# Optimization experiments

Hardware: AMD Instinct MI355X
Metric: run time of the kernel (lower is better)

## Reference

```python
import jax, jax.numpy as jnp
import numpy as np

H = 8          # num heads
LN_EPS = 1e-5  # torch LayerNorm default

_SHAPES = {
    'src': (1024, 8, 256), 'pos': (1024, 8, 256), 'query_embed': (80, 8, 256), 'cam_mask': (8, 80, 1024),
    'enc_qkv_w': (2, 768, 256), 'enc_qkv_b': (2, 768), 'enc_out_w': (2, 256, 256), 'enc_out_b': (2, 256),
    'enc_ln1_g': (2, 256), 'enc_ln1_b': (2, 256),
    'enc_ff1_w': (2, 2048, 256), 'enc_ff1_b': (2, 2048), 'enc_ff2_w': (2, 256, 2048), 'enc_ff2_b': (2, 256),
    'enc_ln2_g': (2, 256), 'enc_ln2_b': (2, 256),
    'dec_sa_qkv_w': (2, 768, 256), 'dec_sa_qkv_b': (2, 768), 'dec_sa_out_w': (2, 256, 256), 'dec_sa_out_b': (2, 256),
    'dec_ln1_g': (2, 256), 'dec_ln1_b': (2, 256),
    'dec_ca_qkv_w': (2, 768, 256), 'dec_ca_qkv_b': (2, 768), 'dec_ca_out_w': (2, 256, 256), 'dec_ca_out_b': (2, 256),
    'dec_ln2_g': (2, 256), 'dec_ln2_b': (2, 256),
    'dec_ff1_w': (2, 2048, 256), 'dec_ff1_b': (2, 2048), 'dec_ff2_w': (2, 256, 2048), 'dec_ff2_b': (2, 256),
    'dec_ln3_g': (2, 256), 'dec_ln3_b': (2, 256),
    'dec_norm_g': (256,), 'dec_norm_b': (256,),
}


def setup_inputs() -> dict:
    key = jax.random.key(0)
    out = {}
    for i, (name, sh) in enumerate(_SHAPES.items()):
        k = jax.random.fold_in(key, i)
        if name.endswith('_g'):
            out[name] = jnp.ones(sh, jnp.float32)
        elif name.endswith('ln1_b') or name.endswith('ln2_b') or name.endswith('ln3_b') or name == 'dec_norm_b':
            out[name] = jnp.zeros(sh, jnp.float32)
        else:
            scale = 1.0 if name in ('src', 'pos', 'query_embed', 'cam_mask') else 0.02
            out[name] = jax.random.normal(k, sh, dtype=jnp.float32) * scale
    return out


def layer_norm(x, g, b):
    mu = jnp.mean(x, axis=-1, keepdims=True)
    var = jnp.mean(jnp.square(x - mu), axis=-1, keepdims=True)
    return (x - mu) * jax.lax.rsqrt(var + LN_EPS) * g + b


def mha(q_in, k_in, v_in, qkv_w, qkv_b, out_w, out_b, bias=None):
    # q_in: [L,B,D], k_in/v_in: [S,B,D]; torch layout: projections are x @ W.T + b
    L, B, D = q_in.shape
    S = k_in.shape[0]
    hd = D // H
    wq, wk, wv = qkv_w[:D], qkv_w[D:2 * D], qkv_w[2 * D:]
    bq, bk, bv = qkv_b[:D], qkv_b[D:2 * D], qkv_b[2 * D:]
    q = (q_in @ wq.T + bq).reshape(L, B, H, hd).transpose(1, 2, 0, 3)  # [B,H,L,hd]
    k = (k_in @ wk.T + bk).reshape(S, B, H, hd).transpose(1, 2, 0, 3)  # [B,H,S,hd]
    v = (v_in @ wv.T + bv).reshape(S, B, H, hd).transpose(1, 2, 0, 3)
    logits = jnp.einsum('bhld,bhsd->bhls', q, k) * (1.0 / np.sqrt(hd))
    if bias is not None:
        logits = logits + bias[:, None, :, :]  # CAM bias broadcast over heads
    attn = jax.nn.softmax(logits, axis=-1)
    o = jnp.einsum('bhls,bhsd->bhld', attn, v).transpose(2, 0, 1, 3).reshape(L, B, D)
    return o @ out_w.T + out_b


def reference(src, pos, query_embed, cam_mask,
              enc_qkv_w, enc_qkv_b, enc_out_w, enc_out_b, enc_ln1_g, enc_ln1_b,
              enc_ff1_w, enc_ff1_b, enc_ff2_w, enc_ff2_b, enc_ln2_g, enc_ln2_b,
              dec_sa_qkv_w, dec_sa_qkv_b, dec_sa_out_w, dec_sa_out_b, dec_ln1_g, dec_ln1_b,
              dec_ca_qkv_w, dec_ca_qkv_b, dec_ca_out_w, dec_ca_out_b, dec_ln2_g, dec_ln2_b,
              dec_ff1_w, dec_ff1_b, dec_ff2_w, dec_ff2_b, dec_ln3_g, dec_ln3_b,
              dec_norm_g, dec_norm_b):
    n_enc = enc_qkv_w.shape[0]
    n_dec = dec_sa_qkv_w.shape[0]
    # --- encoder (post-norm DETR style, pos added to q,k) ---
    mem = src
    for i in range(n_enc):
        qk = mem + pos
        a = mha(qk, qk, mem, enc_qkv_w[i], enc_qkv_b[i], enc_out_w[i], enc_out_b[i])
        mem = layer_norm(mem + a, enc_ln1_g[i], enc_ln1_b[i])
        f = jax.nn.relu(mem @ enc_ff1_w[i].T + enc_ff1_b[i]) @ enc_ff2_w[i].T + enc_ff2_b[i]
        mem = layer_norm(mem + f, enc_ln2_g[i], enc_ln2_b[i])
    # --- decoder: tgt starts at zeros (Q2L), query_embed is query_pos ---
    tgt = jnp.zeros_like(query_embed)
    for i in range(n_dec):
        qk = tgt + query_embed
        sa = mha(qk, qk, tgt, dec_sa_qkv_w[i], dec_sa_qkv_b[i], dec_sa_out_w[i], dec_sa_out_b[i])
        tgt = layer_norm(tgt + sa, dec_ln1_g[i], dec_ln1_b[i])
        ca = mha(tgt + query_embed, mem + pos, mem,
                 dec_ca_qkv_w[i], dec_ca_qkv_b[i], dec_ca_out_w[i], dec_ca_out_b[i],
                 bias=cam_mask)  # MA: CAM-derived additive attention bias [B,L,S]
        tgt = layer_norm(tgt + ca, dec_ln2_g[i], dec_ln2_b[i])
        f = jax.nn.relu(tgt @ dec_ff1_w[i].T + dec_ff1_b[i]) @ dec_ff2_w[i].T + dec_ff2_b[i]
        tgt = layer_norm(tgt + f, dec_ln3_g[i], dec_ln3_b[i])
    out = layer_norm(tgt, dec_norm_g, dec_norm_b)
    return out[None]  # [1, L, B, D] as in TransformerDecoder's output.unsqueeze(0)
```

## Files before the change

kernel.cpp:

```cpp
#include <hip/hip_runtime.h>
#include <hip/hip_bf16.h>
#include <cstdint>
#include <cstddef>

typedef __hip_bfloat16 bf16;
typedef float f4 __attribute__((ext_vector_type(4)));
typedef float f32x4 __attribute__((ext_vector_type(4)));
typedef short s8v __attribute__((ext_vector_type(8)));
typedef unsigned short u16x4 __attribute__((ext_vector_type(4)));

#define LN_EPS 1e-5f

__device__ __forceinline__ void async_cp16(const void* g, void* lds) {
  __builtin_amdgcn_global_load_lds(
      (const __attribute__((address_space(1))) unsigned int*)g,
      (__attribute__((address_space(3))) unsigned int*)lds, 16, 0, 0);
}

#define NCAST 11
struct CastArgs {
  const float* in[NCAST];
  bf16* out[NCAST];
  int end4[NCAST];
  int nseg;
};

__global__ __launch_bounds__(256) void cast_multi(CastArgs a, int total4) {
  int i = blockIdx.x * 256 + threadIdx.x;
  if (i >= total4) return;
  int s = 0;
  while (i >= a.end4[s]) ++s;
  int j = i - (s ? a.end4[s - 1] : 0);
  f4 v = ((const f4*)a.in[s])[j];
  u16x4 o;
#pragma unroll
  for (int c = 0; c < 4; ++c) {
    bf16 h = __float2bfloat16(v[c]);
    o[c] = *reinterpret_cast<unsigned short*>(&h);
  }
  ((u16x4*)a.out[s])[j] = o;
}

__global__ __launch_bounds__(256) void add_bf16_kernel(const float* __restrict__ a,
                                                       const float* __restrict__ b,
                                                       bf16* __restrict__ out, int n4) {
  int i = blockIdx.x * 256 + threadIdx.x;
  if (i < n4) {
    f4 x = ((const f4*)a)[i];
    f4 y = ((const f4*)b)[i];
    u16x4 o;
#pragma unroll
    for (int j = 0; j < 4; ++j) {
      bf16 h = __float2bfloat16(x[j] + y[j]);
      o[j] = *reinterpret_cast<unsigned short*>(&h);
    }
    ((u16x4*)out)[i] = o;
  }
}

template <int TB, int MODE, int SPLITK>
__global__ __launch_bounds__(256, 2) void mfma_gemm(
    const bf16* __restrict__ A, const bf16* __restrict__ W,
    const float* __restrict__ bias, float* __restrict__ C,
    bf16* __restrict__ Cb, int M, int N, int K, int HL) {
  constexpr int WM = TB / 2, WN = TB / 2;
  constexpr int MR = WM / 16, NR = WN / 16;
  constexpr int NCH = TB / 32;
  __shared__ __attribute__((aligned(16))) unsigned short As[TB][64];
  __shared__ __attribute__((aligned(16))) unsigned short Ws[TB][64];
  const int tid = threadIdx.x;
  const int lane = tid & 63, wave = tid >> 6;
  const int wr = wave >> 1, wc = wave & 1;
  const int bm = blockIdx.x * TB, bn = blockIdx.y * TB;
  const int fr = lane & 15, fo = lane >> 4;
  const int srowi = lane >> 3;
  const int slot = lane & 7;
  const int gcol = (slot ^ srowi) * 8;

  const int kchunk = K / SPLITK;
  const int kbeg = (SPLITK > 1) ? blockIdx.z * kchunk : 0;

  f32x4 acc[MR][NR] = {};

  for (int k0 = kbeg; k0 < kbeg + kchunk; k0 += 64) {
    __syncthreads();
#pragma unroll
    for (int c = 0; c < NCH; ++c) {
      int rbase = wave * (TB / 4) + c * 8;
      int row = rbase + srowi;
      async_cp16(A + (size_t)(bm + row) * K + k0 + gcol, &As[rbase][0]);
      async_cp16(W + (size_t)(bn + row) * K + k0 + gcol, &Ws[rbase][0]);
    }
    __syncthreads();
#pragma unroll
    for (int ks = 0; ks < 2; ++ks) {
      s8v a[MR], b[NR];
#pragma unroll
      for (int mi = 0; mi < MR; ++mi) {
        int row = wr * WM + mi * 16 + fr;
        a[mi] = *(const s8v*)((const char*)&As[0][0] + row * 128 +
                              ((ks * 64 + fo * 16) ^ ((row & 7) << 4)));
      }
#pragma unroll
      for (int ni = 0; ni < NR; ++ni) {
        int row = wc * WN + ni * 16 + fr;
        b[ni] = *(const s8v*)((const char*)&Ws[0][0] + row * 128 +
                              ((ks * 64 + fo * 16) ^ ((row & 7) << 4)));
      }
#pragma unroll
      for (int mi = 0; mi < MR; ++mi)
#pragma unroll
        for (int ni = 0; ni < NR; ++ni)
          acc[mi][ni] = __builtin_amdgcn_mfma_f32_16x16x32_bf16(
              a[mi], b[ni], acc[mi][ni], 0, 0, 0);
    }
  }

  const int r0 = (lane >> 4) * 4;
  float* Cz = (MODE == 4) ? C + (size_t)blockIdx.z * M * N : C;
#pragma unroll
  for (int mi = 0; mi < MR; ++mi) {
#pragma unroll
    for (int ni = 0; ni < NR; ++ni) {
      int col = bn + wc * WN + ni * 16 + fr;
      float bv = (MODE == 4) ? 0.f : bias[col];
#pragma unroll
      for (int r = 0; r < 4; ++r) {
        int row = bm + wr * WM + mi * 16 + r0 + r;
        float t = acc[mi][ni][r] + bv;
        if (MODE == 2) t = fmaxf(t, 0.f);
        if (MODE == 0) {
          C[(size_t)row * N + col] = t;
        } else if (MODE == 4) {
          Cz[(size_t)row * N + col] = t;
        } else if (MODE == 3) {
          int l = row >> 3, bb = row & 7;
          int sec = col >> 8, hh = (col >> 5) & 7, d = col & 31;
          Cb[(size_t)sec * ((size_t)64 * HL * 32) +
             ((size_t)(bb * 8 + hh) * HL + l) * 32 + d] = __float2bfloat16(t);
        } else {
          Cb[(size_t)row * N + col] = __float2bfloat16(t);
        }
      }
    }
  }
}

template <int HAS_BIAS, int PARTIAL>
__global__ __launch_bounds__(256) void attn_mfma(
    const bf16* __restrict__ Qh, const bf16* __restrict__ Kh,
    const bf16* __restrict__ Vh, const float* __restrict__ bias,
    bf16* __restrict__ O, float* __restrict__ PO, float* __restrict__ PM,
    float* __restrict__ PL, int L, int S, int SC, float scale) {
  __shared__ __attribute__((aligned(16))) unsigned short Ks[64][40];
  __shared__ __attribute__((aligned(16))) unsigned short Vt[32][88];
  __shared__ __attribute__((aligned(16))) unsigned short Ps[4][16][72];
  const int tid = threadIdx.x;
  const int lane = tid & 63, wave = tid >> 6;
  const int fr = lane & 15, fo = lane >> 4;
  const int bh = blockIdx.y;
  const int b = bh >> 3, h = bh & 7;
  const int q0 = blockIdx.x * 64 + wave * 16;

  const int cz = PARTIAL ? blockIdx.z : 0;
  const int sb = PARTIAL ? cz * SC : 0;
  const int se = PARTIAL ? min(S, sb + SC) : S;

  s8v qf = {};
  if (q0 + fr < L)
    qf = *(const s8v*)(Qh + ((size_t)bh * L + q0 + fr) * 32 + fo * 8);

  float m[4] = {-1e30f, -1e30f, -1e30f, -1e30f};
  float lsum[4] = {};
  f32x4 oacc[2] = {};

  const int srow = tid & 63, sco = (tid >> 6) * 8;
  const int qrow_base = q0 + fo * 4;

  s8v kvN = {}, vvN = {};
  auto load_tile = [&](int s0) {
    s8v kv = {}, vv = {};
    if (s0 + srow < se) {
      size_t so = ((size_t)bh * S + s0 + srow) * 32 + sco;
      kv = *(const s8v*)(Kh + so);
      vv = *(const s8v*)(Vh + so);
    }
    kvN = kv; vvN = vv;
  };
  auto store_tile = [&]() {
    *(s8v*)&Ks[srow][sco] = kvN;
#pragma unroll
    for (int j = 0; j < 8; ++j)
      Vt[sco + j][srow] = ((unsigned short*)&vvN)[j];
  };

  load_tile(sb);
  store_tile();
  __syncthreads();

  for (int s0 = sb; s0 < se; s0 += 64) {
    const bool more = (s0 + 64 < se);
    if (more) load_tile(s0 + 64);

    f32x4 sa[4];
#pragma unroll
    for (int kb = 0; kb < 4; ++kb) {
      s8v bf = *(const s8v*)&Ks[kb * 16 + fr][fo * 8];
      f32x4 z = {};
      sa[kb] = __builtin_amdgcn_mfma_f32_16x16x32_bf16(qf, bf, z, 0, 0, 0);
    }

    float lg[4][4];
#pragma unroll
    for (int kb = 0; kb < 4; ++kb) {
      int key = s0 + kb * 16 + fr;
      bool kok = key < se;
#pragma unroll
      for (int r = 0; r < 4; ++r) {
        float t = sa[kb][r] * scale;
        if (HAS_BIAS) {
          int q = qrow_base + r;
          int qc = q < L ? q : L - 1;
          t += bias[((size_t)b * L + qc) * S + key];
        }
        lg[kb][r] = kok ? t : -1e30f;
      }
    }

    float tm[4];
#pragma unroll
    for (int r = 0; r < 4; ++r)
      tm[r] = fmaxf(fmaxf(lg[0][r], lg[1][r]), fmaxf(lg[2][r], lg[3][r]));
#pragma unroll
    for (int off = 1; off <= 8; off <<= 1)
#pragma unroll
      for (int r = 0; r < 4; ++r)
        tm[r] = fmaxf(tm[r], __shfl_xor(tm[r], off, 64));

    float pr[4][4];
#pragma unroll
    for (int r = 0; r < 4; ++r) {
      float nm = fmaxf(m[r], tm[r]);
      float rs = __expf(m[r] - nm);
      m[r] = nm;
      lsum[r] *= rs;
      oacc[0][r] *= rs;
      oacc[1][r] *= rs;
      float ps = 0.f;
#pragma unroll
      for (int kb = 0; kb < 4; ++kb) {
        float p = __expf(lg[kb][r] - nm);
        pr[kb][r] = p;
        ps += p;
      }
      lsum[r] += ps;
    }

#pragma unroll
    for (int kb = 0; kb < 4; ++kb)
#pragma unroll
      for (int r = 0; r < 4; ++r) {
        bf16 hp = __float2bfloat16(pr[kb][r]);
        Ps[wave][fo * 4 + r][kb * 16 + fr] = *(unsigned short*)&hp;
      }

#pragma unroll
    for (int ks = 0; ks < 2; ++ks) {
      s8v af = *(const s8v*)&Ps[wave][fr][ks * 32 + fo * 8];
#pragma unroll
      for (int dh = 0; dh < 2; ++dh) {
        s8v vf = *(const s8v*)&Vt[dh * 16 + fr][ks * 32 + fo * 8];
        oacc[dh] = __builtin_amdgcn_mfma_f32_16x16x32_bf16(af, vf, oacc[dh], 0, 0, 0);
      }
    }

    if (more) {
      __syncthreads();
      store_tile();
      __syncthreads();
    }
  }

#pragma unroll
  for (int off = 1; off <= 8; off <<= 1)
#pragma unroll
    for (int r = 0; r < 4; ++r)
      lsum[r] += __shfl_xor(lsum[r], off, 64);

#pragma unroll
  for (int r = 0; r < 4; ++r) {
    int q = qrow_base + r;
    if (q < L) {
      if (PARTIAL) {
        size_t pi = ((size_t)cz * 64 + bh) * L + q;
        float* po = PO + pi * 32;
        po[fr] = oacc[0][r];
        po[16 + fr] = oacc[1][r];
        if (fr == 0) { PM[pi] = m[r]; PL[pi] = lsum[r]; }
      } else {
        float inv = 1.f / lsum[r];
        bf16* op = O + ((size_t)q * 8 + b) * 256 + h * 32;
        op[fr] = __float2bfloat16(oacc[0][r] * inv);
        op[16 + fr] = __float2bfloat16(oacc[1][r] * inv);
      }
    }
  }
}

__global__ __launch_bounds__(256) void attn_combine(
    const float* __restrict__ PO, const float* __restrict__ PM,
    const float* __restrict__ PL, bf16* __restrict__ O, int L, int NC) {
  int gid = blockIdx.x * 256 + threadIdx.x;
  if (gid >= 64 * L * 32) return;
  int d = gid & 31;
  int rem = gid >> 5;
  int q = rem % L, bh = rem / L;
  int b = bh >> 3, h = bh & 7;
  float M = -1e30f;
  for (int c = 0; c < NC; ++c) M = fmaxf(M, PM[((size_t)c * 64 + bh) * L + q]);
  float lsum = 0.f, o = 0.f;
  for (int c = 0; c < NC; ++c) {
    size_t pi = ((size_t)c * 64 + bh) * L + q;
    float w = __expf(PM[pi] - M);
    lsum += PL[pi] * w;
    o += PO[pi * 32 + d] * w;
  }
  O[((size_t)q * 8 + b) * 256 + h * 32 + d] = __float2bfloat16(o / lsum);
}

__global__ __launch_bounds__(256) void ln_kernel(
    const float* __restrict__ x, const float* __restrict__ res,
    const float* __restrict__ parts, int nparts, int pstride,
    const float* __restrict__ gbias,
    const float* __restrict__ g, const float* __restrict__ b,
    float* __restrict__ out, bf16* __restrict__ outb) {
  const int row = blockIdx.x, tid = threadIdx.x;
  size_t idx = (size_t)row * 256 + tid;
  float v = x[idx];
  if (res) v += res[idx];
  if (parts) {
    for (int z = 0; z < nparts; ++z) v += parts[(size_t)z * pstride + idx];
  }
  if (gbias) v += gbias[tid];
  float s = v, s2 = v * v;
#pragma unroll
  for (int off = 32; off >= 1; off >>= 1) {
    s += __shfl_down(s, off);
    s2 += __shfl_down(s2, off);
  }
  __shared__ float red[8];
  int wv = tid >> 6;
  if ((tid & 63) == 0) { red[wv] = s; red[4 + wv] = s2; }
  __syncthreads();
  if (tid == 0) {
    float ts = red[0] + red[1] + red[2] + red[3];
    float ts2 = red[4] + red[5] + red[6] + red[7];
    float mu = ts * (1.f / 256.f);
    float var = ts2 * (1.f / 256.f) - mu * mu;
    red[0] = mu;
    red[1] = rsqrtf(var + LN_EPS);
  }
  __syncthreads();
  float y = (v - red[0]) * red[1] * g[tid] + b[tid];
  if (out) out[idx] = y;
  if (outb) outb[idx] = __float2bfloat16(y);
}

extern "C" void kernel_launch(void* const* d_in, const int* in_sizes, int n_in,
                              void* d_out, int out_size, void* d_ws, size_t ws_size,
                              hipStream_t stream) {
  const float* src         = (const float*)d_in[0];
  const float* pos         = (const float*)d_in[1];
  const float* query_embed = (const float*)d_in[2];
  const float* cam_mask    = (const float*)d_in[3];
  const float* enc_qkv_w   = (const float*)d_in[4];
  const float* enc_qkv_b   = (const float*)d_in[5];
  const float* enc_out_w   = (const float*)d_in[6];
  const float* enc_out_b   = (const float*)d_in[7];
  const float* enc_ln1_g   = (const float*)d_in[8];
  const float* enc_ln1_b   = (const float*)d_in[9];
  const float* enc_ff1_w   = (const float*)d_in[10];
  const float* enc_ff1_b   = (const float*)d_in[11];
  const float* enc_ff2_w   = (const float*)d_in[12];
  const float* enc_ff2_b   = (const float*)d_in[13];
  const float* enc_ln2_g   = (const float*)d_in[14];
  const float* enc_ln2_b   = (const float*)d_in[15];
  const float* dec_sa_qkv_w= (const float*)d_in[16];
  const float* dec_sa_qkv_b= (const float*)d_in[17];
  const float* dec_sa_out_w= (const float*)d_in[18];
  const float* dec_sa_out_b= (const float*)d_in[19];
  const float* dec_ln1_g   = (const float*)d_in[20];
  const float* dec_ln1_b   = (const float*)d_in[21];
  const float* dec_ca_qkv_w= (const float*)d_in[22];
  const float* dec_ca_qkv_b= (const float*)d_in[23];
  const float* dec_ca_out_w= (const float*)d_in[24];
  const float* dec_ca_out_b= (const float*)d_in[25];
  const float* dec_ln2_g   = (const float*)d_in[26];
  const float* dec_ln2_b   = (const float*)d_in[27];
  const float* dec_ff1_w   = (const float*)d_in[28];
  const float* dec_ff1_b   = (const float*)d_in[29];
  const float* dec_ff2_w   = (const float*)d_in[30];
  const float* dec_ff2_b   = (const float*)d_in[31];
  const float* dec_ln3_g   = (const float*)d_in[32];
  const float* dec_ln3_b   = (const float*)d_in[33];
  const float* dec_norm_g  = (const float*)d_in[34];
  const float* dec_norm_b  = (const float*)d_in[35];

  size_t off = 0;
  char* base = (char*)d_ws;
  auto af = [&](size_t n) { float* p = (float*)(base + off); off += n * 4; return p; };
  auto ab = [&](size_t n) { bf16*  p = (bf16*)(base + off);  off += n * 2; return p; };

  float* mem  = af(2097152);
  float* r1   = af(2097152);
  float* PO   = af(8388608);
  float* pm   = af(262144);
  float* pl   = af(262144);
  float* tgt  = af(163840);
  float* tpr  = af(163840);
  bf16* memb  = ab(2097152);
  bf16* qkb   = ab(2097152);
  bf16* aob   = ab(2097152);
  bf16* ffb   = ab(16777216);
  bf16* bufQ  = ab(4194304);
  bf16* bufK  = ab(2097152);
  bf16* bufV  = ab(2097152);
  bf16* tgtb  = ab(163840);
  bf16* tqkb  = ab(163840);
  bf16* taob  = ab(163840);
  bf16* tffb  = ab(1310720);
  bf16* w_enc_qkv = ab(393216);
  bf16* w_enc_out = ab(131072);
  bf16* w_enc_ff1 = ab(1048576);
  bf16* w_enc_ff2 = ab(1048576);
  bf16* w_sa_qkv  = ab(393216);
  bf16* w_sa_out  = ab(131072);
  bf16* w_ca_qkv  = ab(393216);
  bf16* w_ca_out  = ab(131072);
  bf16* w_dec_ff1 = ab(1048576);
  bf16* w_dec_ff2 = ab(1048576);

  const float scale = 0.17677669529663687f;

  {
    CastArgs ca;
    const float* ins[NCAST] = {enc_qkv_w, enc_out_w, enc_ff1_w, enc_ff2_w,
                               dec_sa_qkv_w, dec_sa_out_w, dec_ca_qkv_w,
                               dec_ca_out_w, dec_ff1_w, dec_ff2_w, src};
    bf16* outs[NCAST] = {w_enc_qkv, w_enc_out, w_enc_ff1, w_enc_ff2,
                         w_sa_qkv, w_sa_out, w_ca_qkv,
                         w_ca_out, w_dec_ff1, w_dec_ff2, memb};
    int n4s[NCAST] = {98304, 32768, 262144, 262144, 98304, 32768, 98304,
                      32768, 262144, 262144, 524288};
    int acc = 0;
    for (int s = 0; s < NCAST; ++s) {
      ca.in[s] = ins[s]; ca.out[s] = outs[s];
      acc += n4s[s]; ca.end4[s] = acc;
    }
    ca.nseg = NCAST;
    cast_multi<<<(acc + 255) / 256, 256, 0, stream>>>(ca, acc);
  }
  hipMemcpyAsync(mem, src, (size_t)2097152 * 4, hipMemcpyDeviceToDevice, stream);

  auto g64_f = [&](const bf16* A, const bf16* W, const float* bias, float* C,
                   int M, int N, int K) {
    mfma_gemm<64, 0, 1><<<dim3(M / 64, N / 64), 256, 0, stream>>>(
        A, W, bias, C, nullptr, M, N, K, 0);
  };
  auto g64_head = [&](const bf16* A, const bf16* W, const float* bias, bf16* Cb,
                      int M, int N, int K, int HL) {
    mfma_gemm<64, 3, 1><<<dim3(M / 64, N / 64), 256, 0, stream>>>(
        A, W, bias, nullptr, Cb, M, N, K, HL);
  };
  auto g64_relu = [&](const bf16* A, const bf16* W, const float* bias, bf16* Cb,
                      int M, int N, int K) {
    mfma_gemm<64, 2, 1><<<dim3(M / 64, N / 64), 256, 0, stream>>>(
        A, W, bias, nullptr, Cb, M, N, K, 0);
  };
  auto g128_relu = [&](const bf16* A, const bf16* W, const float* bias, bf16* Cb,
                       int M, int N, int K) {
    mfma_gemm<128, 2, 1><<<dim3(M / 128, N / 128), 256, 0, stream>>>(
        A, W, bias, nullptr, Cb, M, N, K, 0);
  };

  for (int i = 0; i < 2; ++i) {
    const bf16* wq = w_enc_qkv + (size_t)i * 196608;
    const float* qkvb = enc_qkv_b + (size_t)i * 768;
    add_bf16_kernel<<<2048, 256, 0, stream>>>(mem, pos, qkb, 524288);
    g64_head(qkb, wq, qkvb, bufQ, 8192, 512, 256, 1024);
    g64_head(memb, wq + 131072, qkvb + 512, bufV, 8192, 256, 256, 1024);
    attn_mfma<0, 0><<<dim3(16, 64), 256, 0, stream>>>(
        bufQ, bufQ + 2097152, bufV, nullptr, aob, nullptr, nullptr, nullptr,
        1024, 1024, 0, scale);
    g64_f(aob, w_enc_out + (size_t)i * 65536, enc_out_b + i * 256, r1,
          8192, 256, 256);
    ln_kernel<<<8192, 256, 0, stream>>>(mem, r1, nullptr, 0, 0, nullptr,
                                        enc_ln1_g + i * 256, enc_ln1_b + i * 256,
                                        mem, memb);
    g128_relu(memb, w_enc_ff1 + (size_t)i * 524288, enc_ff1_b + i * 2048, ffb,
              8192, 2048, 256);
    mfma_gemm<128, 4, 4><<<dim3(64, 2, 4), 256, 0, stream>>>(
        ffb, w_enc_ff2 + (size_t)i * 524288, nullptr, PO, nullptr,
        8192, 256, 2048, 0);
    ln_kernel<<<8192, 256, 0, stream>>>(mem, nullptr, PO, 4, 2097152,
                                        enc_ff2_b + i * 256,
                                        enc_ln2_g + i * 256, enc_ln2_b + i * 256,
                                        mem, memb);
  }

  hipMemsetAsync(tgt, 0, (size_t)163840 * 4, stream);
  hipMemsetAsync(tgtb, 0, (size_t)163840 * 2, stream);
  add_bf16_kernel<<<2048, 256, 0, stream>>>(mem, pos, qkb, 524288);

  for (int i = 0; i < 2; ++i) {
    const bf16* wsa = w_sa_qkv + (size_t)i * 196608;
    const float* sab = dec_sa_qkv_b + (size_t)i * 768;
    const bf16* wca = w_ca_qkv + (size_t)i * 196608;
    const float* cab = dec_ca_qkv_b + (size_t)i * 768;

    add_bf16_kernel<<<160, 256, 0, stream>>>(tgt, query_embed, tqkb, 40960);
    g64_head(tqkb, wsa, sab, bufQ, 640, 512, 256, 80);
    g64_head(tgtb, wsa + 131072, sab + 512, bufV, 640, 256, 256, 80);
    attn_mfma<0, 0><<<dim3(2, 64), 256, 0, stream>>>(
        bufQ, bufQ + 163840, bufV, nullptr, taob, nullptr, nullptr, nullptr,
        80, 80, 0, scale);
    g64_f(taob, w_sa_out + (size_t)i * 65536, dec_sa_out_b + i * 256, tpr,
          640, 256, 256);
    ln_kernel<<<640, 256, 0, stream>>>(tgt, tpr, nullptr, 0, 0, nullptr,
                                       dec_ln1_g + i * 256, dec_ln1_b + i * 256,
                                       tgt, tgtb);
    add_bf16_kernel<<<160, 256, 0, stream>>>(tgt, query_embed, tqkb, 40960);
    g64_head(tqkb, wca, cab, bufQ, 640, 256, 256, 80);
    g64_head(qkb, wca + 65536, cab + 256, bufK, 8192, 256, 256, 1024);
    g64_head(memb, wca + 131072, cab + 512, bufV, 8192, 256, 256, 1024);
    attn_mfma<1, 1><<<dim3(2, 64, 8), 256, 0, stream>>>(
        bufQ, bufK, bufV, cam_mask, nullptr, PO, pm, pl,
        80, 1024, 128, scale);
    attn_combine<<<640, 256, 0, stream>>>(PO, pm, pl, taob, 80, 8);
    g64_f(taob, w_ca_out + (size_t)i * 65536, dec_ca_out_b + i * 256, tpr,
          640, 256, 256);
    ln_kernel<<<640, 256, 0, stream>>>(tgt, tpr, nullptr, 0, 0, nullptr,
                                       dec_ln2_g + i * 256, dec_ln2_b + i * 256,
                                       tgt, tgtb);
    g64_relu(tgtb, w_dec_ff1 + (size_t)i * 524288, dec_ff1_b + i * 2048, tffb,
             640, 2048, 256);
    mfma_gemm<64, 4, 4><<<dim3(10, 4, 4), 256, 0, stream>>>(
        tffb, w_dec_ff2 + (size_t)i * 524288, nullptr, PO, nullptr,
        640, 256, 2048, 0);
    ln_kernel<<<640, 256, 0, stream>>>(tgt, nullptr, PO, 4, 163840,
                                       dec_ff2_b + i * 256,
                                       dec_ln3_g + i * 256, dec_ln3_b + i * 256,
                                       tgt, tgtb);
  }

  ln_kernel<<<640, 256, 0, stream>>>(tgt, nullptr, nullptr, 0, 0, nullptr,
                                     dec_norm_g, dec_norm_b,
                                     (float*)d_out, nullptr);
}
```

Before: 433.5 us.

## Rework attention: transposed V layout, LDS-free K/V loads, log2-domain softmax

The V projection now writes head-transposed output, so the attention kernel reads K and V fragments straight from global memory into registers instead of staging them through LDS with block-level syncs. Scores are computed transposed (K as the A operand), and the softmax scale and log2(e) are folded into the Q projection epilogue and a pre-scaled copy of cam_mask, so exp2f replaces __expf. A lazy rescale skips the running-max correction unless the max grows by more than 8. Bias reads become vectorised float4 loads and outputs are stored as packed writes. The grid axes are swapped, occupancy bounds are raised, and an extra scale kernel and buffer are added per call.

```diff
diff --git a/kernel.cpp b/kernel.cpp
--- a/kernel.cpp
+++ b/kernel.cpp
@@ -10,11 +10,17 @@
 typedef unsigned short u16x4 __attribute__((ext_vector_type(4)));
 
 #define LN_EPS 1e-5f
+#define LOG2E 1.4426950408889634f
 
 __device__ __forceinline__ void async_cp16(const void* g, void* lds) {
   __builtin_amdgcn_global_load_lds(
       (const __attribute__((address_space(1))) unsigned int*)g,
       (__attribute__((address_space(3))) unsigned int*)lds, 16, 0, 0);
+}
+
+__device__ __forceinline__ uint32_t pkbf(float lo, float hi) {
+  bf16 a = __float2bfloat16(lo), c = __float2bfloat16(hi);
+  return (uint32_t)*(unsigned short*)&a | ((uint32_t)*(unsigned short*)&c << 16);
 }
 
 #define NCAST 11
@@ -41,6 +47,16 @@
   ((u16x4*)a.out[s])[j] = o;
 }
 
+__global__ __launch_bounds__(256) void scale_f32_kernel(const float* __restrict__ in,
+                                                        float* __restrict__ out,
+                                                        float s, int n4) {
+  int i = blockIdx.x * 256 + threadIdx.x;
+  if (i < n4) {
+    f4 v = ((const f4*)in)[i];
+    ((f4*)out)[i] = v * s;
+  }
+}
+
 __global__ __launch_bounds__(256) void add_bf16_kernel(const float* __restrict__ a,
                                                        const float* __restrict__ b,
                                                        bf16* __restrict__ out, int n4) {
@@ -62,7 +78,7 @@
 __global__ __launch_bounds__(256, 2) void mfma_gemm(
     const bf16* __restrict__ A, const bf16* __restrict__ W,
     const float* __restrict__ bias, float* __restrict__ C,
-    bf16* __restrict__ Cb, int M, int N, int K, int HL) {
+    bf16* __restrict__ Cb, int M, int N, int K, int HL, float qscale) {
   constexpr int WM = TB / 2, WN = TB / 2;
   constexpr int MR = WM / 16, NR = WN / 16;
   constexpr int NCH = TB / 32;
@@ -136,8 +152,13 @@
         } else if (MODE == 3) {
           int l = row >> 3, bb = row & 7;
           int sec = col >> 8, hh = (col >> 5) & 7, d = col & 31;
+          if (sec == 0) t *= qscale;
           Cb[(size_t)sec * ((size_t)64 * HL * 32) +
              ((size_t)(bb * 8 + hh) * HL + l) * 32 + d] = __float2bfloat16(t);
+        } else if (MODE == 5) {
+          int l = row >> 3, bb = row & 7;
+          int hh = (col >> 5) & 7, d = col & 31;
+          Cb[((size_t)(bb * 8 + hh) * 32 + d) * HL + l] = __float2bfloat16(t);
         } else {
           Cb[(size_t)row * N + col] = __float2bfloat16(t);
         }
@@ -147,161 +168,156 @@
 }
 
 template <int HAS_BIAS, int PARTIAL>
-__global__ __launch_bounds__(256) void attn_mfma(
+__global__ __launch_bounds__(256, 4) void attn_mfma(
     const bf16* __restrict__ Qh, const bf16* __restrict__ Kh,
-    const bf16* __restrict__ Vh, const float* __restrict__ bias,
+    const bf16* __restrict__ VhT, const float* __restrict__ bias,
     bf16* __restrict__ O, float* __restrict__ PO, float* __restrict__ PM,
-    float* __restrict__ PL, int L, int S, int SC, float scale) {
-  __shared__ __attribute__((aligned(16))) unsigned short Ks[64][40];
-  __shared__ __attribute__((aligned(16))) unsigned short Vt[32][88];
-  __shared__ __attribute__((aligned(16))) unsigned short Ps[4][16][72];
+    float* __restrict__ PL, int L, int S, int SC) {
+  __shared__ __attribute__((aligned(16))) uint32_t Ps2[4][16][36];
   const int tid = threadIdx.x;
   const int lane = tid & 63, wave = tid >> 6;
   const int fr = lane & 15, fo = lane >> 4;
-  const int bh = blockIdx.y;
+  const int bh = blockIdx.x;
   const int b = bh >> 3, h = bh & 7;
-  const int q0 = blockIdx.x * 64 + wave * 16;
+  const int q0 = blockIdx.y * 64 + wave * 16;
+  const int q = q0 + fr;
 
   const int cz = PARTIAL ? blockIdx.z : 0;
   const int sb = PARTIAL ? cz * SC : 0;
   const int se = PARTIAL ? min(S, sb + SC) : S;
 
   s8v qf = {};
-  if (q0 + fr < L)
-    qf = *(const s8v*)(Qh + ((size_t)bh * L + q0 + fr) * 32 + fo * 8);
-
-  float m[4] = {-1e30f, -1e30f, -1e30f, -1e30f};
-  float lsum[4] = {};
+  if (q < L) qf = *(const s8v*)(Qh + ((size_t)bh * L + q) * 32 + fo * 8);
+
+  const float* brow = nullptr;
+  if (HAS_BIAS) brow = bias + ((size_t)b * L + (q < L ? q : L - 1)) * S;
+
+  float m = -1e30f, lsum = 0.f;
   f32x4 oacc[2] = {};
 
-  const int srow = tid & 63, sco = (tid >> 6) * 8;
-  const int qrow_base = q0 + fo * 4;
-
-  s8v kvN = {}, vvN = {};
-  auto load_tile = [&](int s0) {
-    s8v kv = {}, vv = {};
-    if (s0 + srow < se) {
-      size_t so = ((size_t)bh * S + s0 + srow) * 32 + sco;
-      kv = *(const s8v*)(Kh + so);
-      vv = *(const s8v*)(Vh + so);
-    }
-    kvN = kv; vvN = vv;
-  };
-  auto store_tile = [&]() {
-    *(s8v*)&Ks[srow][sco] = kvN;
-#pragma unroll
-    for (int j = 0; j < 8; ++j)
-      Vt[sco + j][srow] = ((unsigned short*)&vvN)[j];
-  };
-
-  load_tile(sb);
-  store_tile();
-  __syncthreads();
+  s8v kf[4];
+#pragma unroll
+  for (int kb = 0; kb < 4; ++kb)
+    kf[kb] = *(const s8v*)(Kh + ((size_t)bh * S + sb + kb * 16 + fr) * 32 + fo * 8);
 
   for (int s0 = sb; s0 < se; s0 += 64) {
     const bool more = (s0 + 64 < se);
-    if (more) load_tile(s0 + 64);
+    s8v kn[4];
+    if (more) {
+#pragma unroll
+      for (int kb = 0; kb < 4; ++kb)
+        kn[kb] = *(const s8v*)(Kh + ((size_t)bh * S + s0 + 64 + kb * 16 + fr) * 32 + fo * 8);
+    }
+    s8v vf[2][2];
+#pragma unroll
+    for (int dh = 0; dh < 2; ++dh)
+#pragma unroll
+      for (int ks = 0; ks < 2; ++ks)
+        vf[dh][ks] = *(const s8v*)(VhT + ((size_t)bh * 32 + dh * 16 + fr) * S +
+                                   s0 + ks * 32 + fo * 8);
+    f4 bias4[4];
+    if (HAS_BIAS) {
+#pragma unroll
+      for (int kb = 0; kb < 4; ++kb)
+        bias4[kb] = *(const f4*)(brow + s0 + kb * 16 + 4 * fo);
+    }
 
     f32x4 sa[4];
 #pragma unroll
     for (int kb = 0; kb < 4; ++kb) {
-      s8v bf = *(const s8v*)&Ks[kb * 16 + fr][fo * 8];
       f32x4 z = {};
-      sa[kb] = __builtin_amdgcn_mfma_f32_16x16x32_bf16(qf, bf, z, 0, 0, 0);
-    }
-
-    float lg[4][4];
+      sa[kb] = __builtin_amdgcn_mfma_f32_16x16x32_bf16(kf[kb], qf, z, 0, 0, 0);
+    }
+
+    float lg[16];
+#pragma unroll
+    for (int kb = 0; kb < 4; ++kb)
+#pragma unroll
+      for (int r = 0; r < 4; ++r)
+        lg[kb * 4 + r] = HAS_BIAS ? sa[kb][r] + bias4[kb][r] : sa[kb][r];
+
+    if (s0 + 64 > se) {
+#pragma unroll
+      for (int kb = 0; kb < 4; ++kb)
+#pragma unroll
+        for (int r = 0; r < 4; ++r)
+          if (s0 + kb * 16 + 4 * fo + r >= se) lg[kb * 4 + r] = -1e30f;
+    }
+
+    float tm = lg[0];
+#pragma unroll
+    for (int i = 1; i < 16; ++i) tm = fmaxf(tm, lg[i]);
+    tm = fmaxf(tm, __shfl_xor(tm, 16));
+    tm = fmaxf(tm, __shfl_xor(tm, 32));
+
+    if (__any(tm > m + 8.f)) {
+      float nm = fmaxf(m, tm);
+      float rs = exp2f(m - nm);
+      m = nm;
+      lsum *= rs;
+#pragma unroll
+      for (int r = 0; r < 4; ++r) { oacc[0][r] *= rs; oacc[1][r] *= rs; }
+    }
+
+    float pr[16];
+    float ps = 0.f;
+#pragma unroll
+    for (int i = 0; i < 16; ++i) {
+      pr[i] = exp2f(lg[i] - m);
+      ps += pr[i];
+    }
+    lsum += ps;
+
 #pragma unroll
     for (int kb = 0; kb < 4; ++kb) {
-      int key = s0 + kb * 16 + fr;
-      bool kok = key < se;
-#pragma unroll
-      for (int r = 0; r < 4; ++r) {
-        float t = sa[kb][r] * scale;
-        if (HAS_BIAS) {
-          int q = qrow_base + r;
-          int qc = q < L ? q : L - 1;
-          t += bias[((size_t)b * L + qc) * S + key];
-        }
-        lg[kb][r] = kok ? t : -1e30f;
+      uint32_t w0 = pkbf(pr[kb * 4 + 0], pr[kb * 4 + 1]);
+      uint32_t w1 = pkbf(pr[kb * 4 + 2], pr[kb * 4 + 3]);
+      uint64_t w = (uint64_t)w0 | ((uint64_t)w1 << 32);
+      *(uint64_t*)&Ps2[wave][fr][kb * 8 + 2 * fo] = w;
+    }
+
+    s8v pf[2];
+#pragma unroll
+    for (int ks = 0; ks < 2; ++ks)
+      pf[ks] = *(const s8v*)&Ps2[wave][fr][ks * 16 + 4 * fo];
+
+#pragma unroll
+    for (int dh = 0; dh < 2; ++dh)
+#pragma unroll
+      for (int ks = 0; ks < 2; ++ks)
+        oacc[dh] = __builtin_amdgcn_mfma_f32_16x16x32_bf16(
+            vf[dh][ks], pf[ks], oacc[dh], 0, 0, 0);
+
+    if (more) {
+#pragma unroll
+      for (int kb = 0; kb < 4; ++kb) kf[kb] = kn[kb];
+    }
+  }
+
+  lsum += __shfl_xor(lsum, 16);
+  lsum += __shfl_xor(lsum, 32);
+
+  if (q < L) {
+    if (PARTIAL) {
+      size_t pi = ((size_t)cz * 64 + bh) * L + q;
+      float* po = PO + pi * 32;
+#pragma unroll
+      for (int dh = 0; dh < 2; ++dh) {
+        f4 t;
+#pragma unroll
+        for (int r = 0; r < 4; ++r) t[r] = oacc[dh][r];
+        *(f4*)(po + dh * 16 + 4 * fo) = t;
       }
-    }
-
-    float tm[4];
-#pragma unroll
-    for (int r = 0; r < 4; ++r)
-      tm[r] = fmaxf(fmaxf(lg[0][r], lg[1][r]), fmaxf(lg[2][r], lg[3][r]));
-#pragma unroll
-    for (int off = 1; off <= 8; off <<= 1)
-#pragma unroll
-      for (int r = 0; r < 4; ++r)
-        tm[r] = fmaxf(tm[r], __shfl_xor(tm[r], off, 64));
-
-    float pr[4][4];
-#pragma unroll
-    for (int r = 0; r < 4; ++r) {
-      float nm = fmaxf(m[r], tm[r]);
-      float rs = __expf(m[r] - nm);
-      m[r] = nm;
-      lsum[r] *= rs;
-      oacc[0][r] *= rs;
-      oacc[1][r] *= rs;
-      float ps = 0.f;
-#pragma unroll
-      for (int kb = 0; kb < 4; ++kb) {
-        float p = __expf(lg[kb][r] - nm);
-        pr[kb][r] = p;
-        ps += p;
-      }
-      lsum[r] += ps;
-    }
-
-#pragma unroll
-    for (int kb = 0; kb < 4; ++kb)
-#pragma unroll
-      for (int r = 0; r < 4; ++r) {
-        bf16 hp = __float2bfloat16(pr[kb][r]);
-        Ps[wave][fo * 4 + r][kb * 16 + fr] = *(unsigned short*)&hp;
-      }
-
-#pragma unroll
-    for (int ks = 0; ks < 2; ++ks) {
-      s8v af = *(const s8v*)&Ps[wave][fr][ks * 32 + fo * 8];
+      if (fo == 0) { PM[pi] = m; PL[pi] = lsum; }
+    } else {
+      float inv = 1.f / lsum;
+      bf16* op = O + ((size_t)q * 8 + b) * 256 + h * 32;
 #pragma unroll
       for (int dh = 0; dh < 2; ++dh) {
-        s8v vf = *(const s8v*)&Vt[dh * 16 + fr][ks * 32 + fo * 8];
-        oacc[dh] = __builtin_amdgcn_mfma_f32_16x16x32_bf16(af, vf, oacc[dh], 0, 0, 0);
-      }
-    }
-
-    if (more) {
-      __syncthreads();
-      store_tile();
-      __syncthreads();
-    }
-  }
-
-#pragma unroll
-  for (int off = 1; off <= 8; off <<= 1)
-#pragma unroll
-    for (int r = 0; r < 4; ++r)
-      lsum[r] += __shfl_xor(lsum[r], off, 64);
-
-#pragma unroll
-  for (int r = 0; r < 4; ++r) {
-    int q = qrow_base + r;
-    if (q < L) {
-      if (PARTIAL) {
-        size_t pi = ((size_t)cz * 64 + bh) * L + q;
-        float* po = PO + pi * 32;
-        po[fr] = oacc[0][r];
-        po[16 + fr] = oacc[1][r];
-        if (fr == 0) { PM[pi] = m[r]; PL[pi] = lsum[r]; }
-      } else {
-        float inv = 1.f / lsum[r];
-        bf16* op = O + ((size_t)q * 8 + b) * 256 + h * 32;
-        op[fr] = __float2bfloat16(oacc[0][r] * inv);
-        op[16 + fr] = __float2bfloat16(oacc[1][r] * inv);
+        uint32_t w0 = pkbf(oacc[dh][0] * inv, oacc[dh][1] * inv);
+        uint32_t w1 = pkbf(oacc[dh][2] * inv, oacc[dh][3] * inv);
+        *(uint32_t*)(op + dh * 16 + 4 * fo) = w0;
+        *(uint32_t*)(op + dh * 16 + 4 * fo + 2) = w1;
       }
     }
   }
@@ -321,7 +337,7 @@
   float lsum = 0.f, o = 0.f;
   for (int c = 0; c < NC; ++c) {
     size_t pi = ((size_t)c * 64 + bh) * L + q;
-    float w = __expf(PM[pi] - M);
+    float w = exp2f(PM[pi] - M);
     lsum += PL[pi] * w;
     o += PO[pi * 32 + d] * w;
   }
@@ -416,6 +432,7 @@
   float* PO   = af(8388608);
   float* pm   = af(262144);
   float* pl   = af(262144);
+  float* cmlog= af(655360);
   float* tgt  = af(163840);
   float* tpr  = af(163840);
   bf16* memb  = ab(2097152);
@@ -440,7 +457,7 @@
   bf16* w_dec_ff1 = ab(1048576);
   bf16* w_dec_ff2 = ab(1048576);
 
-  const float scale = 0.17677669529663687f;
+  const float qscale = 0.17677669529663687f * LOG2E;
 
   {
     CastArgs ca;
@@ -460,38 +477,44 @@
     ca.nseg = NCAST;
     cast_multi<<<(acc + 255) / 256, 256, 0, stream>>>(ca, acc);
   }
+  scale_f32_kernel<<<640, 256, 0, stream>>>(cam_mask, cmlog, LOG2E, 163840);
   hipMemcpyAsync(mem, src, (size_t)2097152 * 4, hipMemcpyDeviceToDevice, stream);
 
   auto g64_f = [&](const bf16* A, const bf16* W, const float* bias, float* C,
                    int M, int N, int K) {
     mfma_gemm<64, 0, 1><<<dim3(M / 64, N / 64), 256, 0, stream>>>(
-        A, W, bias, C, nullptr, M, N, K, 0);
+        A, W, bias, C, nullptr, M, N, K, 0, 1.f);
   };
   auto g64_head = [&](const bf16* A, const bf16* W, const float* bias, bf16* Cb,
-                      int M, int N, int K, int HL) {
+                      int M, int N, int K, int HL, float qs) {
     mfma_gemm<64, 3, 1><<<dim3(M / 64, N / 64), 256, 0, stream>>>(
-        A, W, bias, nullptr, Cb, M, N, K, HL);
+        A, W, bias, nullptr, Cb, M, N, K, HL, qs);
+  };
+  auto g64_headT = [&](const bf16* A, const bf16* W, const float* bias, bf16* Cb,
+                       int M, int N, int K, int HL) {
+    mfma_gemm<64, 5, 1><<<dim3(M / 64, N / 64), 256, 0, stream>>>(
+        A, W, bias, nullptr, Cb, M, N, K, HL, 1.f);
   };
   auto g64_relu = [&](const bf16* A, const bf16* W, const float* bias, bf16* Cb,
                       int M, int N, int K) {
     mfma_gemm<64, 2, 1><<<dim3(M / 64, N / 64), 256, 0, stream>>>(
-        A, W, bias, nullptr, Cb, M, N, K, 0);
+        A, W, bias, nullptr, Cb, M, N, K, 0, 1.f);
   };
   auto g128_relu = [&](const bf16* A, const bf16* W, const float* bias, bf16* Cb,
                        int M, int N, int K) {
     mfma_gemm<128, 2, 1><<<dim3(M / 128, N / 128), 256, 0, stream>>>(
-        A, W, bias, nullptr, Cb, M, N, K, 0);
+        A, W, bias, nullptr, Cb, M, N, K, 0, 1.f);
   };
 
   for (int i = 0; i < 2; ++i) {
     const bf16* wq = w_enc_qkv + (size_t)i * 196608;
     const float* qkvb = enc_qkv_b + (size_t)i * 768;
     add_bf16_kernel<<<2048, 256, 0, stream>>>(mem, pos, qkb, 524288);
-    g64_head(qkb, wq, qkvb, bufQ, 8192, 512, 256, 1024);
-    g64_head(memb, wq + 131072, qkvb + 512, bufV, 8192, 256, 256, 1024);
-    attn_mfma<0, 0><<<dim3(16, 64), 256, 0, stream>>>(
+    g64_head(qkb, wq, qkvb, bufQ, 8192, 512, 256, 1024, qscale);
+    g64_headT(memb, wq + 131072, qkvb + 512, bufV, 8192, 256, 256, 1024);
+    attn_mfma<0, 0><<<dim3(64, 16), 256, 0, stream>>>(
         bufQ, bufQ + 2097152, bufV, nullptr, aob, nullptr, nullptr, nullptr,
-        1024, 1024, 0, scale);
+        1024, 1024, 0);
     g64_f(aob, w_enc_out + (size_t)i * 65536, enc_out_b + i * 256, r1,
           8192, 256, 256);
     ln_kernel<<<8192, 256, 0, stream>>>(mem, r1, nullptr, 0, 0, nullptr,
@@ -501,7 +524,7 @@
               8192, 2048, 256);
     mfma_gemm<128, 4, 4><<<dim3(64, 2, 4), 256, 0, stream>>>(
         ffb, w_enc_ff2 + (size_t)i * 524288, nullptr, PO, nullptr,
-        8192, 256, 2048, 0);
+        8192, 256, 2048, 0, 1.f);
     ln_kernel<<<8192, 256, 0, stream>>>(mem, nullptr, PO, 4, 2097152,
                                         enc_ff2_b + i * 256,
                                         enc_ln2_g + i * 256, enc_ln2_b + i * 256,
@@ -519,23 +542,22 @@
     const float* cab = dec_ca_qkv_b + (size_t)i * 768;
 
     add_bf16_kernel<<<160, 256, 0, stream>>>(tgt, query_embed, tqkb, 40960);
-    g64_head(tqkb, wsa, sab, bufQ, 640, 512, 256, 80);
-    g64_head(tgtb, wsa + 131072, sab + 512, bufV, 640, 256, 256, 80);
-    attn_mfma<0, 0><<<dim3(2, 64), 256, 0, stream>>>(
+    g64_head(tqkb, wsa, sab, bufQ, 640, 512, 256, 80, qscale);
+    g64_headT(tgtb, wsa + 131072, sab + 512, bufV, 640, 256, 256, 80);
+    attn_mfma<0, 0><<<dim3(64, 2), 256, 0, stream>>>(
         bufQ, bufQ + 163840, bufV, nullptr, taob, nullptr, nullptr, nullptr,
-        80, 80, 0, scale);
+        80, 80, 0);
     g64_f(taob, w_sa_out + (size_t)i * 65536, dec_sa_out_b + i * 256, tpr,
           640, 256, 256);
     ln_kernel<<<640, 256, 0, stream>>>(tgt, tpr, nullptr, 0, 0, nullptr,
                                        dec_ln1_g + i * 256, dec_ln1_b + i * 256,
                                        tgt, tgtb);
     add_bf16_kernel<<<160, 256, 0, stream>>>(tgt, query_embed, tqkb, 40960);
-    g64_head(tqkb, wca, cab, bufQ, 640, 256, 256, 80);
-    g64_head(qkb, wca + 65536, cab + 256, bufK, 8192, 256, 256, 1024);
-    g64_head(memb, wca + 131072, cab + 512, bufV, 8192, 256, 256, 1024);
-    attn_mfma<1, 1><<<dim3(2, 64, 8), 256, 0, stream>>>(
-        bufQ, bufK, bufV, cam_mask, nullptr, PO, pm, pl,
-        80, 1024, 128, scale);
+    g64_head(tqkb, wca, cab, bufQ, 640, 256, 256, 80, qscale);
+    g64_head(qkb, wca + 65536, cab + 256, bufK, 8192, 256, 256, 1024, 1.f);
+    g64_headT(memb, wca + 131072, cab + 512, bufV, 8192, 256, 256, 1024);
+    attn_mfma<1, 1><<<dim3(64, 2, 8), 256, 0, stream>>>(
+        bufQ, bufK, bufV, cmlog, nullptr, PO, pm, pl, 80, 1024, 128);
     attn_combine<<<640, 256, 0, stream>>>(PO, pm, pl, taob, 80, 8);
     g64_f(taob, w_ca_out + (size_t)i * 65536, dec_ca_out_b + i * 256, tpr,
           640, 256, 256);
@@ -546,7 +568,7 @@
              640, 2048, 256);
     mfma_gemm<64, 4, 4><<<dim3(10, 4, 4), 256, 0, stream>>>(
         tffb, w_dec_ff2 + (size_t)i * 524288, nullptr, PO, nullptr,
-        640, 256, 2048, 0);
+        640, 256, 2048, 0, 1.f);
     ln_kernel<<<640, 256, 0, stream>>>(tgt, nullptr, PO, 4, 163840,
                                        dec_ff2_b + i * 256,
                                        dec_ln3_g + i * 256, dec_ln3_b + i * 256,
```

Result: slower. 462.0 us (+6.6%).
